# Performance work log

Hardware: AMD Instinct MI355X
Metric: run time of the kernel (lower is better)

## Reference

```python
import jax, jax.numpy as jnp
import numpy as np

EPS = 1e-5

def _ada_ln(x, c, W_ss, b_ss):
    # LayerNorm without affine, then conditional scale/bias from c via SiLU->Linear
    mu = jnp.mean(x, axis=-1, keepdims=True)
    var = jnp.mean((x - mu) ** 2, axis=-1, keepdims=True)
    h = (x - mu) / jnp.sqrt(var + EPS)
    ss = jax.nn.silu(c) @ W_ss + b_ss            # [B, 2H]
    scale, bias = jnp.split(ss, 2, axis=-1)      # [B, H] each
    return (1.0 + scale)[:, None, :] * h + bias[:, None, :]

def setup_inputs() -> dict:
    key = jax.random.key(0)
    ks = jax.random.split(key, 12)
    B, Lq, Lkv, H = 8, 2048, 512, 1024
    s = 0.02
    return {
        "x_q": jax.random.normal(ks[0], (B, Lq, H), jnp.float32),
        "x_kv": jax.random.normal(ks[1], (B, Lkv, H), jnp.float32),
        "t_vec": jax.random.normal(ks[2], (B, H), jnp.float32),
        "Wq": jax.random.normal(ks[3], (H, H), jnp.float32) * s,
        "bq": jnp.zeros((H,), jnp.float32),
        "Wkv": jax.random.normal(ks[4], (H, 2 * H), jnp.float32) * s,
        "bkv": jnp.zeros((2 * H,), jnp.float32),
        "Wp": jax.random.normal(ks[5], (H, H), jnp.float32) * s,
        "bp": jnp.zeros((H,), jnp.float32),
        "Wss_q": jax.random.normal(ks[6], (H, 2 * H), jnp.float32) * s,
        "bss_q": jnp.zeros((2 * H,), jnp.float32),
        "Wss_kv": jax.random.normal(ks[7], (H, 2 * H), jnp.float32) * s,
        "bss_kv": jnp.zeros((2 * H,), jnp.float32),
    }

def reference(x_q, x_kv, t_vec, Wq, bq, Wkv, bkv, Wp, bp, Wss_q, bss_q, Wss_kv, bss_kv):
    B, Lq, H = x_q.shape
    Lkv = x_kv.shape[1]
    nh = 16
    dh = H // nh

    xq = _ada_ln(x_q, t_vec, Wss_q, bss_q)
    xkv = _ada_ln(x_kv, t_vec, Wss_kv, bss_kv)

    q = (xq @ Wq + bq).reshape(B, Lq, nh, dh)          # [B,Lq,h,d]
    kv = (xkv @ Wkv + bkv).reshape(B, Lkv, 2, nh, dh)
    k = kv[:, :, 0]                                     # [B,Lkv,h,d]
    v = kv[:, :, 1]

    scores = jnp.einsum("bqhd,bkhd->bhqk", q, k) / jnp.sqrt(jnp.float32(dh))
    attn = jax.nn.softmax(scores, axis=-1)
    out = jnp.einsum("bhqk,bkhd->bqhd", attn, v).reshape(B, Lq, H)
    return x_q + (out @ Wp + bp)
```

## Files before the change

kernel.cpp:

```cpp
#include <hip/hip_runtime.h>
#include <hip/hip_bf16.h>
#include <stdint.h>

typedef __attribute__((ext_vector_type(8))) short bf16x8;
typedef __attribute__((ext_vector_type(4))) float f32x4;
typedef __attribute__((ext_vector_type(4))) _Float16 f16x4;
typedef __attribute__((ext_vector_type(8))) _Float16 f16x8;
typedef __attribute__((ext_vector_type(4))) unsigned short u16x4;

__device__ __forceinline__ float b2f(unsigned short u){
  union { unsigned int i; float f; } x; x.i = ((unsigned int)u) << 16; return x.f;
}
__device__ __forceinline__ unsigned short f2b(float f){
  union { float f; unsigned int i; } x; x.f = f;
  unsigned int r = x.i + 0x7fffu + ((x.i >> 16) & 1u);
  return (unsigned short)(r >> 16);
}

__device__ __forceinline__ void gld_lds16(const void* g, void* l){
  __builtin_amdgcn_global_load_lds((const __attribute__((address_space(1))) unsigned int*)g,
                                   (__attribute__((address_space(3))) unsigned int*)l,
                                   16, 0, 0);
}

__global__ __launch_bounds__(256) void transpose_k(const float* __restrict__ in,
                                                   unsigned short* __restrict__ out,
                                                   int R, int C){
  __shared__ unsigned short tile[32][33];
  int tx = threadIdx.x & 31, ty = threadIdx.x >> 5;
  int r0 = blockIdx.y * 32, c0 = blockIdx.x * 32;
#pragma unroll
  for (int t = 0; t < 4; ++t)
    tile[ty + t*8][tx] = f2b(in[(size_t)(r0 + ty + t*8) * C + c0 + tx]);
  __syncthreads();
#pragma unroll
  for (int t = 0; t < 4; ++t)
    out[(size_t)(c0 + ty + t*8) * R + r0 + tx] = tile[tx][ty + t*8];
}

__global__ __launch_bounds__(256) void ss_init_k(const float* __restrict__ bssq,
                                                 const float* __restrict__ bssk,
                                                 float* __restrict__ ss_q,
                                                 float* __restrict__ ss_kv){
  int idx = blockIdx.x*256 + threadIdx.x;
  int which = idx >> 14, rem = idx & 16383;
  int j = rem & 2047;
  if (which) ss_kv[rem] = bssk[j];
  else       ss_q[rem]  = bssq[j];
}

__global__ __launch_bounds__(256) void ss2_k(const float* __restrict__ tvec,
                                             const float* __restrict__ Wssq,
                                             const float* __restrict__ Wssk,
                                             float* __restrict__ ss_q,
                                             float* __restrict__ ss_kv){
  const int which = blockIdx.z;
  const float* W = which ? Wssk : Wssq;
  float* ss = which ? ss_kv : ss_q;
  const int col = blockIdx.x*256 + threadIdx.x;
  const int k0 = blockIdx.y*64;

  __shared__ float sl[8][64];
  int idx = threadIdx.x;
#pragma unroll
  for (int t = 0; t < 2; ++t){
    int i = idx + t*256;
    int b = i >> 6, k = i & 63;
    float c = tvec[b*1024 + k0 + k];
    sl[b][k] = c / (1.f + __expf(-c));
  }
  __syncthreads();

  float acc[8] = {0.f,0.f,0.f,0.f,0.f,0.f,0.f,0.f};
#pragma unroll 8
  for (int k = 0; k < 64; ++k){
    float w = W[(size_t)(k0 + k)*2048 + col];
#pragma unroll
    for (int b = 0; b < 8; ++b) acc[b] += sl[b][k] * w;
  }
#pragma unroll
  for (int b = 0; b < 8; ++b)
    atomicAdd(&ss[b*2048 + col], acc[b]);
}

__global__ __launch_bounds__(256) void ada_ln_k(const float* __restrict__ x,
                                                const float* __restrict__ ss,
                                                unsigned short* __restrict__ out,
                                                int L){
  int row = blockIdx.x;
  int b = row / L;
  const float* xr = x + (size_t)row * 1024;
  int tid = threadIdx.x;
  float4 v = *(const float4*)&xr[tid*4];
  float s = v.x + v.y + v.z + v.w;
  __shared__ float red[4];
#pragma unroll
  for (int o = 32; o > 0; o >>= 1) s += __shfl_xor(s, o, 64);
  if ((tid & 63) == 0) red[tid >> 6] = s;
  __syncthreads();
  float mu = (red[0]+red[1]+red[2]+red[3]) * (1.f/1024.f);
  __syncthreads();
  float vs = (v.x-mu)*(v.x-mu) + (v.y-mu)*(v.y-mu) + (v.z-mu)*(v.z-mu) + (v.w-mu)*(v.w-mu);
#pragma unroll
  for (int o = 32; o > 0; o >>= 1) vs += __shfl_xor(vs, o, 64);
  if ((tid & 63) == 0) red[tid >> 6] = vs;
  __syncthreads();
  float var = (red[0]+red[1]+red[2]+red[3]) * (1.f/1024.f);
  float inv = rsqrtf(var + 1e-5f);
  const float* sb = ss + (size_t)b*2048;
  float4 sc = *(const float4*)&sb[tid*4];
  float4 bi = *(const float4*)&sb[1024 + tid*4];
  u16x4 o4;
  o4[0] = f2b((1.f + sc.x) * ((v.x-mu)*inv) + bi.x);
  o4[1] = f2b((1.f + sc.y) * ((v.y-mu)*inv) + bi.y);
  o4[2] = f2b((1.f + sc.z) * ((v.z-mu)*inv) + bi.z);
  o4[3] = f2b((1.f + sc.w) * ((v.w-mu)*inv) + bi.w);
  *(u16x4*)&out[(size_t)row*1024 + tid*4] = o4;
}

__global__ __launch_bounds__(256) void gemm_bt_k(const unsigned short* __restrict__ A,
                                                 const unsigned short* __restrict__ BT,
                                                 const float* __restrict__ bias,
                                                 const float* __restrict__ resf,
                                                 unsigned short* __restrict__ Cb,
                                                 float* __restrict__ Cf,
                                                 _Float16* __restrict__ vT,
                                                 int M, int N, int K, int mode){
  __shared__ __attribute__((aligned(16))) unsigned short As[128*64];
  __shared__ __attribute__((aligned(16))) unsigned short Bs[128*64];
  const int tid = threadIdx.x;
  const int wave = tid >> 6, lane = tid & 63;
  const int lm = lane & 15, quad = lane >> 4;

  const int gx = gridDim.x;
  const int nwg = gx * gridDim.y;
  const int lid = blockIdx.y * gx + blockIdx.x;
  const int chunk = nwg >> 3;
  const int tile = (lid & 7) * chunk + (lid >> 3);
  const int m0 = (tile / gx) * 128, n0 = (tile % gx) * 128;

  const int wm = (wave >> 1) * 64, wn = (wave & 1) * 64;
  f32x4 acc[4][4];
#pragma unroll
  for (int i = 0; i < 4; ++i)
#pragma unroll
    for (int j = 0; j < 4; ++j) acc[i][j] = (f32x4){0.f,0.f,0.f,0.f};

  int rowc[4], colc[4];
#pragma unroll
  for (int r = 0; r < 4; ++r){
    int c = r*256 + tid;
    rowc[r] = c >> 3; colc[r] = (c & 7) * 8;
  }

  for (int k0 = 0; k0 < K; k0 += 64){
    __syncthreads();
#pragma unroll
    for (int r = 0; r < 4; ++r)
      gld_lds16(&A[(size_t)(m0 + rowc[r])*K + k0 + colc[r]], &As[(r*256 + tid)*8]);
#pragma unroll
    for (int r = 0; r < 4; ++r)
      gld_lds16(&BT[(size_t)(n0 + rowc[r])*K + k0 + colc[r]], &Bs[(r*256 + tid)*8]);
    __syncthreads();
#pragma unroll
    for (int ks = 0; ks < 2; ++ks){
      bf16x8 af[4], bfr[4];
#pragma unroll
      for (int i = 0; i < 4; ++i)
        af[i] = *(bf16x8*)&As[(wm + i*16 + lm)*64 + ks*32 + quad*8];
#pragma unroll
      for (int j = 0; j < 4; ++j)
        bfr[j] = *(bf16x8*)&Bs[(wn + j*16 + lm)*64 + ks*32 + quad*8];
#pragma unroll
      for (int i = 0; i < 4; ++i)
#pragma unroll
        for (int j = 0; j < 4; ++j)
          acc[i][j] = __builtin_amdgcn_mfma_f32_16x16x32_bf16(af[i], bfr[j], acc[i][j], 0, 0, 0);
    }
  }

  if (mode == 2 && n0 >= 1024){
#pragma unroll
    for (int j = 0; j < 4; ++j){
      int col = n0 + wn + j*16 + lm;
      int d = col - 1024;
      float bv = bias[col];
#pragma unroll
      for (int i = 0; i < 4; ++i){
        int rowb = m0 + wm + i*16 + quad*4;
        int brow = rowb >> 9, l = rowb & 511;
        f16x4 h4;
#pragma unroll
        for (int p = 0; p < 4; ++p) h4[p] = (_Float16)(acc[i][j][p] + bv);
        *(f16x4*)&vT[((size_t)brow*1024 + d)*512 + l] = h4;
      }
    }
    return;
  }

#pragma unroll
  for (int j = 0; j < 4; ++j){
    int col = n0 + wn + j*16 + lm;
    float bv = bias[col];
#pragma unroll
    for (int i = 0; i < 4; ++i){
#pragma unroll
      for (int p = 0; p < 4; ++p){
        int row = m0 + wm + i*16 + quad*4 + p;
        float v = acc[i][j][p] + bv;
        if (mode == 1){
          Cf[(size_t)row*N + col] = v + resf[(size_t)row*N + col];
        } else {
          Cb[(size_t)row*1024 + col] = f2b(v);
        }
      }
    }
  }
}

__global__ __launch_bounds__(256) void attn_k(const unsigned short* __restrict__ q,
                                              const unsigned short* __restrict__ kbuf,
                                              const _Float16* __restrict__ vT,
                                              unsigned short* __restrict__ out){
  const int lid = (blockIdx.z * gridDim.y + blockIdx.y) * gridDim.x + blockIdx.x;
  const int tile = (lid & 7) * 256 + (lid >> 3);
  const int qb = tile & 15, h = (tile >> 4) & 15, b = tile >> 8;
  const int tid = threadIdx.x;
  const int wave = tid >> 6, lane = tid & 63;
  const int lm = lane & 15, quad = lane >> 4;
  const int q0 = qb * 128;

  __shared__ __attribute__((aligned(16))) unsigned short Ks[64*72];
  __shared__ __attribute__((aligned(16))) _Float16      Vs[64*72];

  bf16x8 qf[2][2];
#pragma unroll
  for (int u = 0; u < 2; ++u){
    const unsigned short* qrow = q + ((size_t)b*2048 + q0 + wave*32 + u*16 + lm)*1024 + h*64;
    qf[u][0] = *(const bf16x8*)&qrow[quad*8];
    qf[u][1] = *(const bf16x8*)&qrow[32 + quad*8];
  }

  const unsigned short* kb = kbuf + ((size_t)b*512)*1024 + h*64;
  const _Float16*       vb = vT + ((size_t)b*1024 + h*64)*512;

  f32x4 oacc[2][4];
#pragma unroll
  for (int u = 0; u < 2; ++u)
#pragma unroll
    for (int nt = 0; nt < 4; ++nt) oacc[u][nt] = (f32x4){0.f,0.f,0.f,0.f};
  float m_run[2] = {-1e30f, -1e30f}, l_run[2] = {0.f, 0.f};

  const int srow = tid >> 3, scol = (tid & 7) * 8;

  for (int kt = 0; kt < 8; ++kt){
    const int l0 = kt * 64;
    __syncthreads();
#pragma unroll
    for (int r = 0; r < 2; ++r){
      int row = r*32 + srow;
      *(bf16x8*)&Ks[row*72 + scol] = *(const bf16x8*)&kb[(size_t)(l0 + row)*1024 + scol];
      *(f16x8*)&Vs[row*72 + scol]  = *(const f16x8*)&vb[(size_t)row*512 + l0 + scol];
    }
    __syncthreads();

    f32x4 sacc[2][4];
#pragma unroll
    for (int u = 0; u < 2; ++u)
#pragma unroll
      for (int s = 0; s < 4; ++s) sacc[u][s] = (f32x4){0.f,0.f,0.f,0.f};
#pragma unroll
    for (int s = 0; s < 4; ++s){
      bf16x8 kf0 = *(bf16x8*)&Ks[(s*16 + lm)*72 + quad*8];
      bf16x8 kf1 = *(bf16x8*)&Ks[(s*16 + lm)*72 + 32 + quad*8];
#pragma unroll
      for (int u = 0; u < 2; ++u){
        sacc[u][s] = __builtin_amdgcn_mfma_f32_16x16x32_bf16(kf0, qf[u][0], sacc[u][s], 0, 0, 0);
        sacc[u][s] = __builtin_amdgcn_mfma_f32_16x16x32_bf16(kf1, qf[u][1], sacc[u][s], 0, 0, 0);
      }
    }

    f16x4 pf[2][4];
#pragma unroll
    for (int u = 0; u < 2; ++u){
      float tm = -1e30f;
#pragma unroll
      for (int s = 0; s < 4; ++s)
#pragma unroll
        for (int p = 0; p < 4; ++p) tm = fmaxf(tm, sacc[u][s][p]);
      tm = fmaxf(tm, __shfl_xor(tm, 16, 64));
      tm = fmaxf(tm, __shfl_xor(tm, 32, 64));
      float m_new = fmaxf(m_run[u], tm * 0.125f);
      float alpha = __expf(m_run[u] - m_new);
      m_run[u] = m_new;
      l_run[u] *= alpha;
      float ap[4];
#pragma unroll
      for (int p = 0; p < 4; ++p) ap[p] = __shfl(alpha, quad*4 + p, 64);
#pragma unroll
      for (int nt = 0; nt < 4; ++nt){
        oacc[u][nt][0] *= ap[0]; oacc[u][nt][1] *= ap[1];
        oacc[u][nt][2] *= ap[2]; oacc[u][nt][3] *= ap[3];
      }
#pragma unroll
      for (int s = 0; s < 4; ++s)
#pragma unroll
        for (int p = 0; p < 4; ++p){
          float e = __expf(sacc[u][s][p] * 0.125f - m_new);
          l_run[u] += e;
          pf[u][s][p] = (_Float16)e;
        }
    }

#pragma unroll
    for (int s = 0; s < 4; ++s){
#pragma unroll
      for (int nt = 0; nt < 4; ++nt){
        f16x4 vf = *(const f16x4*)&Vs[(size_t)(nt*16 + lm)*72 + s*16 + quad*4];
#pragma unroll
        for (int u = 0; u < 2; ++u)
          oacc[u][nt] = __builtin_amdgcn_mfma_f32_16x16x16f16(pf[u][s], vf, oacc[u][nt], 0, 0, 0);
      }
    }
  }

#pragma unroll
  for (int u = 0; u < 2; ++u){
    float lr = l_run[u];
    lr += __shfl_xor(lr, 16, 64);
    lr += __shfl_xor(lr, 32, 64);
    float rinv = 1.f / lr;
    float rp[4];
#pragma unroll
    for (int p = 0; p < 4; ++p) rp[p] = __shfl(rinv, quad*4 + p, 64);
    const size_t obase = ((size_t)b*2048 + q0 + wave*32 + u*16) * 1024 + h*64;
#pragma unroll
    for (int nt = 0; nt < 4; ++nt)
#pragma unroll
      for (int p = 0; p < 4; ++p){
        int row = quad*4 + p;
        out[obase + (size_t)row*1024 + nt*16 + lm] = f2b(oacc[u][nt][p] * rp[p]);
      }
  }
}

extern "C" void kernel_launch(void* const* d_in, const int* in_sizes, int n_in,
                              void* d_out, int out_size, void* d_ws, size_t ws_size,
                              hipStream_t stream){
  const float* x_q  = (const float*)d_in[0];
  const float* x_kv = (const float*)d_in[1];
  const float* tvec = (const float*)d_in[2];
  const float* Wq   = (const float*)d_in[3];
  const float* bq   = (const float*)d_in[4];
  const float* Wkv  = (const float*)d_in[5];
  const float* bkv  = (const float*)d_in[6];
  const float* Wp   = (const float*)d_in[7];
  const float* bp   = (const float*)d_in[8];
  const float* Wssq = (const float*)d_in[9];
  const float* bssq = (const float*)d_in[10];
  const float* Wssk = (const float*)d_in[11];
  const float* bssk = (const float*)d_in[12];

  char* ws = (char*)d_ws;
  float*          ss_q  = (float*)(ws + 0);
  float*          ss_kv = (float*)(ws + 65536);
  unsigned short* xq    = (unsigned short*)(ws + 131072);
  unsigned short* xkv   = (unsigned short*)(ws + 33685504);
  unsigned short* qbuf  = (unsigned short*)(ws + 42074112);
  unsigned short* kbuf  = (unsigned short*)(ws + 75628544);
  _Float16*       vTbuf = (_Float16*)     (ws + 84017152);
  unsigned short* WqT   = (unsigned short*)(ws + 92405760);
  unsigned short* WkvT  = (unsigned short*)(ws + 94502912);
  unsigned short* WpT   = (unsigned short*)(ws + 98697216);

  dim3 blk(256);
  transpose_k<<<dim3(32, 32), blk, 0, stream>>>(Wq,  WqT,  1024, 1024);
  transpose_k<<<dim3(64, 32), blk, 0, stream>>>(Wkv, WkvT, 1024, 2048);
  transpose_k<<<dim3(32, 32), blk, 0, stream>>>(Wp,  WpT,  1024, 1024);

  ss_init_k<<<dim3(128), blk, 0, stream>>>(bssq, bssk, ss_q, ss_kv);
  ss2_k<<<dim3(8, 16, 2), blk, 0, stream>>>(tvec, Wssq, Wssk, ss_q, ss_kv);

  ada_ln_k<<<dim3(16384), blk, 0, stream>>>(x_q,  ss_q,  xq,  2048);
  ada_ln_k<<<dim3(4096),  blk, 0, stream>>>(x_kv, ss_kv, xkv, 512);

  gemm_bt_k<<<dim3(8, 128), blk, 0, stream>>>(xq,  WqT,  bq,  nullptr, qbuf, nullptr, nullptr,
                                              16384, 1024, 1024, 0);
  gemm_bt_k<<<dim3(16, 32), blk, 0, stream>>>(xkv, WkvT, bkv, nullptr, kbuf, nullptr, vTbuf,
                                              4096, 2048, 1024, 2);

  attn_k<<<dim3(16, 16, 8), blk, 0, stream>>>(qbuf, kbuf, vTbuf, xq);

  gemm_bt_k<<<dim3(8, 128), blk, 0, stream>>>(xq, WpT, bp, x_q, nullptr, (float*)d_out, nullptr,
                                              16384, 1024, 1024, 1);
}
```

Measured before the change: 439.8 us.

## Double-buffer GEMM LDS loads and add 256x256 tile GEMM for Q/out projections

Measured after the change: 433.6 us. No clear change (-1.4%).

```diff
diff --git a/kernel.cpp b/kernel.cpp
--- a/kernel.cpp
+++ b/kernel.cpp
@@ -126,8 +126,8 @@
                                                  float* __restrict__ Cf,
                                                  _Float16* __restrict__ vT,
                                                  int M, int N, int K, int mode){
-  __shared__ __attribute__((aligned(16))) unsigned short As[128*64];
-  __shared__ __attribute__((aligned(16))) unsigned short Bs[128*64];
+  __shared__ __attribute__((aligned(16))) unsigned short As[2][128*64];
+  __shared__ __attribute__((aligned(16))) unsigned short Bs[2][128*64];
   const int tid = threadIdx.x;
   const int wave = tid >> 6, lane = tid & 63;
   const int lm = lane & 15, quad = lane >> 4;
@@ -153,31 +153,42 @@
     rowc[r] = c >> 3; colc[r] = (c & 7) * 8;
   }
 
-  for (int k0 = 0; k0 < K; k0 += 64){
-    __syncthreads();
-#pragma unroll
-    for (int r = 0; r < 4; ++r)
-      gld_lds16(&A[(size_t)(m0 + rowc[r])*K + k0 + colc[r]], &As[(r*256 + tid)*8]);
-#pragma unroll
-    for (int r = 0; r < 4; ++r)
-      gld_lds16(&BT[(size_t)(n0 + rowc[r])*K + k0 + colc[r]], &Bs[(r*256 + tid)*8]);
-    __syncthreads();
+#define STAGE128(buf, kk)                                                              \
+  {                                                                                    \
+    _Pragma("unroll")                                                                  \
+    for (int r = 0; r < 4; ++r)                                                        \
+      gld_lds16(&A[(size_t)(m0 + rowc[r])*K + (kk) + colc[r]], &As[buf][(r*256 + tid)*8]); \
+    _Pragma("unroll")                                                                  \
+    for (int r = 0; r < 4; ++r)                                                        \
+      gld_lds16(&BT[(size_t)(n0 + rowc[r])*K + (kk) + colc[r]], &Bs[buf][(r*256 + tid)*8]); \
+  }
+
+  const int NT = K >> 6;
+  STAGE128(0, 0);
+  __syncthreads();
+
+  int cur = 0;
+  for (int t = 0; t < NT; ++t){
+    if (t + 1 < NT) STAGE128(cur ^ 1, (t + 1) << 6);
 #pragma unroll
     for (int ks = 0; ks < 2; ++ks){
       bf16x8 af[4], bfr[4];
 #pragma unroll
       for (int i = 0; i < 4; ++i)
-        af[i] = *(bf16x8*)&As[(wm + i*16 + lm)*64 + ks*32 + quad*8];
+        af[i] = *(bf16x8*)&As[cur][(wm + i*16 + lm)*64 + ks*32 + quad*8];
 #pragma unroll
       for (int j = 0; j < 4; ++j)
-        bfr[j] = *(bf16x8*)&Bs[(wn + j*16 + lm)*64 + ks*32 + quad*8];
+        bfr[j] = *(bf16x8*)&Bs[cur][(wn + j*16 + lm)*64 + ks*32 + quad*8];
 #pragma unroll
       for (int i = 0; i < 4; ++i)
 #pragma unroll
         for (int j = 0; j < 4; ++j)
           acc[i][j] = __builtin_amdgcn_mfma_f32_16x16x32_bf16(af[i], bfr[j], acc[i][j], 0, 0, 0);
     }
-  }
+    __syncthreads();
+    cur ^= 1;
+  }
+#undef STAGE128
 
   if (mode == 2 && n0 >= 1024){
 #pragma unroll
@@ -204,6 +215,98 @@
     float bv = bias[col];
 #pragma unroll
     for (int i = 0; i < 4; ++i){
+#pragma unroll
+      for (int p = 0; p < 4; ++p){
+        int row = m0 + wm + i*16 + quad*4 + p;
+        float v = acc[i][j][p] + bv;
+        if (mode == 1){
+          Cf[(size_t)row*N + col] = v + resf[(size_t)row*N + col];
+        } else {
+          Cb[(size_t)row*1024 + col] = f2b(v);
+        }
+      }
+    }
+  }
+}
+
+__global__ __launch_bounds__(512) void gemm256_k(const unsigned short* __restrict__ A,
+                                                 const unsigned short* __restrict__ BT,
+                                                 const float* __restrict__ bias,
+                                                 const float* __restrict__ resf,
+                                                 unsigned short* __restrict__ Cb,
+                                                 float* __restrict__ Cf,
+                                                 int M, int N, int K, int mode){
+  __shared__ __attribute__((aligned(16))) unsigned short As[2][256*64];
+  __shared__ __attribute__((aligned(16))) unsigned short Bs[2][256*64];
+  const int tid = threadIdx.x;
+  const int wave = tid >> 6, lane = tid & 63;
+  const int lm = lane & 15, quad = lane >> 4;
+
+  const int gx = gridDim.x;
+  const int nwg = gx * gridDim.y;
+  const int lid = blockIdx.y * gx + blockIdx.x;
+  const int chunk = nwg >> 3;
+  const int tile = (lid & 7) * chunk + (lid >> 3);
+  const int m0 = (tile / gx) * 256, n0 = (tile % gx) * 256;
+
+  const int wm = (wave >> 2) * 128, wn = (wave & 3) * 64;
+
+  f32x4 acc[8][4];
+#pragma unroll
+  for (int i = 0; i < 8; ++i)
+#pragma unroll
+    for (int j = 0; j < 4; ++j) acc[i][j] = (f32x4){0.f,0.f,0.f,0.f};
+
+  int rowc[4], colc[4];
+#pragma unroll
+  for (int r = 0; r < 4; ++r){
+    int c = r*512 + tid;
+    rowc[r] = c >> 3; colc[r] = (c & 7) * 8;
+  }
+
+#define STAGE256(buf, kk)                                                              \
+  {                                                                                    \
+    _Pragma("unroll")                                                                  \
+    for (int r = 0; r < 4; ++r)                                                        \
+      gld_lds16(&A[(size_t)(m0 + rowc[r])*K + (kk) + colc[r]], &As[buf][(r*512 + tid)*8]); \
+    _Pragma("unroll")                                                                  \
+    for (int r = 0; r < 4; ++r)                                                        \
+      gld_lds16(&BT[(size_t)(n0 + rowc[r])*K + (kk) + colc[r]], &Bs[buf][(r*512 + tid)*8]); \
+  }
+
+  const int NT = K >> 6;
+  STAGE256(0, 0);
+  __syncthreads();
+
+  int cur = 0;
+  for (int t = 0; t < NT; ++t){
+    if (t + 1 < NT) STAGE256(cur ^ 1, (t + 1) << 6);
+#pragma unroll
+    for (int ks = 0; ks < 2; ++ks){
+      bf16x8 af[8], bfr[4];
+#pragma unroll
+      for (int i = 0; i < 8; ++i)
+        af[i] = *(bf16x8*)&As[cur][(wm + i*16 + lm)*64 + ks*32 + quad*8];
+#pragma unroll
+      for (int j = 0; j < 4; ++j)
+        bfr[j] = *(bf16x8*)&Bs[cur][(wn + j*16 + lm)*64 + ks*32 + quad*8];
+#pragma unroll
+      for (int i = 0; i < 8; ++i)
+#pragma unroll
+        for (int j = 0; j < 4; ++j)
+          acc[i][j] = __builtin_amdgcn_mfma_f32_16x16x32_bf16(af[i], bfr[j], acc[i][j], 0, 0, 0);
+    }
+    __syncthreads();
+    cur ^= 1;
+  }
+#undef STAGE256
+
+#pragma unroll
+  for (int j = 0; j < 4; ++j){
+    int col = n0 + wn + j*16 + lm;
+    float bv = bias[col];
+#pragma unroll
+    for (int i = 0; i < 8; ++i){
 #pragma unroll
       for (int p = 0; p < 4; ++p){
         int row = m0 + wm + i*16 + quad*4 + p;
@@ -384,13 +487,13 @@
   ada_ln_k<<<dim3(16384), blk, 0, stream>>>(x_q,  ss_q,  xq,  2048);
   ada_ln_k<<<dim3(4096),  blk, 0, stream>>>(x_kv, ss_kv, xkv, 512);
 
-  gemm_bt_k<<<dim3(8, 128), blk, 0, stream>>>(xq,  WqT,  bq,  nullptr, qbuf, nullptr, nullptr,
-                                              16384, 1024, 1024, 0);
+  gemm256_k<<<dim3(4, 64), dim3(512), 0, stream>>>(xq, WqT, bq, nullptr, qbuf, nullptr,
+                                                   16384, 1024, 1024, 0);
   gemm_bt_k<<<dim3(16, 32), blk, 0, stream>>>(xkv, WkvT, bkv, nullptr, kbuf, nullptr, vTbuf,
                                               4096, 2048, 1024, 2);
 
   attn_k<<<dim3(16, 16, 8), blk, 0, stream>>>(qbuf, kbuf, vTbuf, xq);
 
-  gemm_bt_k<<<dim3(8, 128), blk, 0, stream>>>(xq, WpT, bp, x_q, nullptr, (float*)d_out, nullptr,
-                                              16384, 1024, 1024, 1);
-}
+  gemm256_k<<<dim3(4, 64), dim3(512), 0, stream>>>(xq, WpT, bp, x_q, nullptr, (float*)d_out,
+                                                   16384, 1024, 1024, 1);
+}
```
